# Kernel optimization log

Hardware: AMD Instinct MI355X
Metric: run time of the kernel (lower is better)

## Reference

```python
import jax, jax.numpy as jnp
import numpy as np

HIDDEN = 128
EDGE_DIM = 32
N_NODES = 50000
N_EDGES = 800000


def setup_inputs() -> dict:
    key = jax.random.key(0)
    ks = jax.random.split(key, 8)
    node_features = jax.random.normal(ks[0], (N_NODES, HIDDEN), dtype=jnp.float32)
    edge_index = jax.random.randint(ks[1], (2, N_EDGES), 0, N_NODES, dtype=jnp.int64)
    edge_attr = jax.random.normal(ks[2], (N_EDGES, EDGE_DIM), dtype=jnp.float32)
    # parameters (Linear stored as [in, out] for x @ W + b)
    s_et = 1.0 / np.sqrt(EDGE_DIM)
    W_edge = jax.random.uniform(ks[3], (EDGE_DIM, HIDDEN), jnp.float32, -s_et, s_et)
    b_edge = jnp.zeros((HIDDEN,), jnp.float32)
    s1 = 1.0 / np.sqrt(3 * HIDDEN)
    W1 = jax.random.uniform(ks[4], (3 * HIDDEN, HIDDEN), jnp.float32, -s1, s1)
    b1 = jnp.zeros((HIDDEN,), jnp.float32)
    s2 = 1.0 / np.sqrt(HIDDEN)
    W2 = jax.random.uniform(ks[5], (HIDDEN, 1), jnp.float32, -s2, s2)
    b2 = jnp.zeros((1,), jnp.float32)
    return {
        "node_features": node_features,
        "edge_attr": edge_attr,
        "W_edge": W_edge, "b_edge": b_edge,
        "W1": W1, "b1": b1, "W2": W2, "b2": b2,
        "edge_index": edge_index,
    }


def reference(node_features, edge_attr, W_edge, b_edge, W1, b1, W2, b2, edge_index):
    row, col = edge_index[0], edge_index[1]
    src = node_features[row]                 # [E, H] gather
    dst = node_features[col]                 # [E, H] gather
    edge_feat = edge_attr @ W_edge + b_edge  # [E, H]
    combined = jnp.concatenate([src, edge_feat, dst], axis=-1)  # [E, 3H]
    h = jax.nn.relu(combined @ W1 + b1)      # [E, H]
    attn = jax.nn.sigmoid(h @ W2 + b2)       # [E, 1]
    return attn
```

## Files before the change

### kernel.cpp

```cpp
#include <hip/hip_runtime.h>
#include <hip/hip_bf16.h>

#define HIDDEN   128
#define EDGE_DIM 32
#define NNODE    50000
#define NEDGE    800000
#define KSTEPS   9
#define NFRAG    8
#define LDS_KS   8

typedef __attribute__((ext_vector_type(4))) float        f32x4;
typedef __attribute__((ext_vector_type(8))) short        bf16x8;
typedef __attribute__((ext_vector_type(4))) unsigned int u32x4;

#define BPACK_USHORTS  (KSTEPS * NFRAG * 64 * 8)
#define BIAS_OFF_BYTES (BPACK_USHORTS * 2)
#define FLAG_OFF_BYTES (BIAS_OFF_BYTES + 128 * 4)
#define NODE_OFF_BYTES 74752
#define IDX_OFF_BYTES  (NODE_OFF_BYTES + NNODE * HIDDEN * 2)
#define WS_NEEDED      (IDX_OFF_BYTES + 2 * NEDGE * 4)

__device__ __forceinline__ unsigned short f2bf(float f) {
  unsigned u = __builtin_bit_cast(unsigned, f);
  u += 0x7FFFu + ((u >> 16) & 1u);
  return (unsigned short)(u >> 16);
}

__device__ __forceinline__ unsigned cvt_pk_bf16(float a, float b) {
  union { __hip_bfloat162 h; unsigned u; } cv;
  cv.h = __float22bfloat162_rn(make_float2(a, b));
  return cv.u;
}

__device__ __forceinline__ bf16x8 pack8(f32x4 lo, f32x4 hi) {
  u32x4 u;
  u[0] = cvt_pk_bf16(lo[0], lo[1]);
  u[1] = cvt_pk_bf16(lo[2], lo[3]);
  u[2] = cvt_pk_bf16(hi[0], hi[1]);
  u[3] = cvt_pk_bf16(hi[2], hi[3]);
  return __builtin_bit_cast(bf16x8, u);
}

__device__ __forceinline__ void gload_lds16(const void* g, void* l) {
  __builtin_amdgcn_global_load_lds(
      (const __attribute__((address_space(1))) unsigned int*)g,
      (__attribute__((address_space(3))) unsigned int*)l, 16, 0, 0);
}

#define MFMA(a, b, c) __builtin_amdgcn_mfma_f32_16x16x32_bf16((a), (b), (c), 0, 0, 0)

__global__ void setup_kernel(const float* __restrict__ W_edge,
                             const float* __restrict__ b_edge,
                             const float* __restrict__ W1,
                             const float* __restrict__ b1,
                             const void*  __restrict__ eidx,
                             unsigned short* __restrict__ Bpack,
                             float* __restrict__ bias_eff,
                             int*   __restrict__ flag64) {
  const int bid = blockIdx.x, tid = threadIdx.x;
  if (bid < 36) {
    const int pair  = bid * 2 + (tid >> 6);
    const int lane  = tid & 63;
    const int kstep = pair >> 3;
    const int f     = pair & 7;
    const int col   = f * 16 + (lane & 15);
    const int kbase = kstep * 32 + (lane >> 4) * 8;
    float vals[8];
#pragma unroll
    for (int j = 0; j < 8; ++j) {
      const int k = kbase + j;
      float val;
      if (k < 128) {
        val = W1[k * 128 + col];
      } else if (k < 256) {
        val = W1[(k + 128) * 128 + col];
      } else {
        const int kk = k - 256;
        float s = 0.f;
        for (int t = 0; t < 128; ++t)
          s = fmaf(W_edge[kk * 128 + t], W1[(128 + t) * 128 + col], s);
        val = s;
      }
      vals[j] = val;
    }
    u32x4 sv;
#pragma unroll
    for (int j = 0; j < 4; ++j)
      sv[j] = (unsigned)f2bf(vals[2 * j]) | ((unsigned)f2bf(vals[2 * j + 1]) << 16);
    *(u32x4*)(Bpack + ((kstep * NFRAG + f) * 64 + lane) * 8) = sv;
  } else {
    if (tid < 128) {
      float s = b1[tid];
      for (int t = 0; t < 128; ++t)
        s = fmaf(b_edge[t], W1[(128 + t) * 128 + tid], s);
      bias_eff[tid] = s;
    }
    if (tid == 0) {
      const unsigned* w = (const unsigned*)eidx;
      int all0 = 1;
      for (int i = 0; i < 64; ++i) all0 &= (w[2 * i + 1] == 0u) ? 1 : 0;
      *flag64 = all0;
    }
  }
}

__global__ __launch_bounds__(256) void cvt_nodes_kernel(const float* __restrict__ nodef,
                                                        unsigned short* __restrict__ nbf) {
  const int i = blockIdx.x * 256 + threadIdx.x;
  if (i >= NNODE * HIDDEN / 8) return;
  f32x4 lo = *(const f32x4*)(nodef + i * 8);
  f32x4 hi = *(const f32x4*)(nodef + i * 8 + 4);
  *(bf16x8*)(nbf + i * 8) = pack8(lo, hi);
}

__global__ __launch_bounds__(256) void cvt_idx_kernel(const void* __restrict__ eidx,
                                                      const int* __restrict__ flag64,
                                                      int* __restrict__ idx32) {
  const int i = blockIdx.x * 256 + threadIdx.x;
  if (i >= 2 * NEDGE) return;
  if (*flag64) idx32[i] = (int)((const long long*)eidx)[i];
  else         idx32[i] = ((const int*)eidx)[i];
}

__global__ __launch_bounds__(256, 2) void edge_attn_kernel(
    const unsigned short* __restrict__ nbf,
    const float* __restrict__ eattr,
    const int*   __restrict__ idx32,
    const unsigned short* __restrict__ Bpack,
    const float* __restrict__ bias_eff,
    const float* __restrict__ W2,
    const float* __restrict__ b2,
    float* __restrict__ out) {
  __shared__ unsigned short lds_b[LDS_KS * NFRAG * 64 * 8];

  const int tid   = threadIdx.x;
  const int lane  = tid & 63;
  const int wid   = tid >> 6;
  const int l15   = lane & 15;
  const int kg    = lane >> 4;
  const int ebase = blockIdx.x * 256 + wid * 64;

#pragma unroll
  for (int i = 0; i < 16; ++i) {
    const char* g = (const char*)Bpack + (size_t)(i * 256 + tid) * 16;
    char*       l = (char*)lds_b + (size_t)(i * 256 + wid * 64) * 16;
    gload_lds16(g, l);
  }

  int r[4], c[4];
#pragma unroll
  for (int mf = 0; mf < 4; ++mf) {
    r[mf] = idx32[ebase + mf * 16 + l15];
    c[mf] = idx32[NEDGE + ebase + mf * 16 + l15];
  }

  bf16x8 a[4][4];
#pragma unroll
  for (int mf = 0; mf < 4; ++mf)
#pragma unroll
    for (int ks = 0; ks < 4; ++ks)
      a[mf][ks] = *(const bf16x8*)(nbf + (size_t)r[mf] * HIDDEN + kg * 8 + ks * 32);

  __syncthreads();

  f32x4 acc[4][NFRAG];
#pragma unroll
  for (int mf = 0; mf < 4; ++mf)
#pragma unroll
    for (int f = 0; f < NFRAG; ++f)
      acc[mf][f] = (f32x4){0.f, 0.f, 0.f, 0.f};

#pragma unroll
  for (int ks = 0; ks < 4; ++ks)
#pragma unroll
    for (int f = 0; f < NFRAG; ++f) {
      bf16x8 bfr = *(const bf16x8*)(lds_b + ((ks * NFRAG + f) * 64 + lane) * 8);
#pragma unroll
      for (int mf = 0; mf < 4; ++mf)
        acc[mf][f] = MFMA(a[mf][ks], bfr, acc[mf][f]);
    }

  __builtin_amdgcn_sched_barrier(0);

#pragma unroll
  for (int mf = 0; mf < 4; ++mf)
#pragma unroll
    for (int ks = 0; ks < 4; ++ks)
      a[mf][ks] = *(const bf16x8*)(nbf + (size_t)c[mf] * HIDDEN + kg * 8 + ks * 32);

#pragma unroll
  for (int ks = 0; ks < 4; ++ks)
#pragma unroll
    for (int f = 0; f < NFRAG; ++f) {
      bf16x8 bfr = *(const bf16x8*)(lds_b + (((ks + 4) * NFRAG + f) * 64 + lane) * 8);
#pragma unroll
      for (int mf = 0; mf < 4; ++mf)
        acc[mf][f] = MFMA(a[mf][ks], bfr, acc[mf][f]);
    }

  __builtin_amdgcn_sched_barrier(0);

  bf16x8 ae[4];
#pragma unroll
  for (int mf = 0; mf < 4; ++mf) {
    const float* pe = eattr + (size_t)(ebase + mf * 16 + l15) * EDGE_DIM + kg * 8;
    f32x4 lo = *(const f32x4*)(pe);
    f32x4 hi = *(const f32x4*)(pe + 4);
    ae[mf] = pack8(lo, hi);
  }
#pragma unroll
  for (int f = 0; f < NFRAG; ++f) {
    bf16x8 bfr = *(const bf16x8*)(Bpack + ((8 * NFRAG + f) * 64 + lane) * 8);
#pragma unroll
    for (int mf = 0; mf < 4; ++mf)
      acc[mf][f] = MFMA(ae[mf], bfr, acc[mf][f]);
  }

  float w2v[NFRAG], bv[NFRAG];
#pragma unroll
  for (int f = 0; f < NFRAG; ++f) {
    w2v[f] = W2[f * 16 + l15];
    bv[f]  = bias_eff[f * 16 + l15];
  }
  const float bias2 = b2[0];

  float part[4][4];
#pragma unroll
  for (int mf = 0; mf < 4; ++mf)
#pragma unroll
    for (int rr = 0; rr < 4; ++rr) {
      float s = 0.f;
#pragma unroll
      for (int f = 0; f < NFRAG; ++f) {
        float h = fmaxf(acc[mf][f][rr] + bv[f], 0.f);
        s = fmaf(h, w2v[f], s);
      }
      part[mf][rr] = s;
    }

#pragma unroll
  for (int mask = 1; mask < 16; mask <<= 1)
#pragma unroll
    for (int mf = 0; mf < 4; ++mf)
#pragma unroll
      for (int rr = 0; rr < 4; ++rr)
        part[mf][rr] += __shfl_xor(part[mf][rr], mask, 64);

  if (l15 == 0) {
#pragma unroll
    for (int mf = 0; mf < 4; ++mf)
#pragma unroll
      for (int rr = 0; rr < 4; ++rr) {
        float x = part[mf][rr] + bias2;
        out[ebase + mf * 16 + kg * 4 + rr] = 1.f / (1.f + __expf(-x));
      }
  }
}

__global__ __launch_bounds__(256) void edge_attn_kernel_fp32(
    const float* __restrict__ nodef,
    const float* __restrict__ eattr,
    const void*  __restrict__ eidx,
    const unsigned short* __restrict__ Bpack,
    const float* __restrict__ bias_eff,
    const float* __restrict__ W2,
    const float* __restrict__ b2,
    const int*   __restrict__ flag64,
    float* __restrict__ out) {
  const int lane  = threadIdx.x & 63;
  const int wid   = threadIdx.x >> 6;
  const int ebase = blockIdx.x * 128 + wid * 32;
  const int l15   = lane & 15;
  const int kg    = lane >> 4;
  const int koff  = kg * 8;
  const int e0 = ebase + l15;
  const int e1 = e0 + 16;

  long r0, c0, r1, c1;
  if (*flag64) {
    const long long* p = (const long long*)eidx;
    r0 = (long)p[e0];          r1 = (long)p[e1];
    c0 = (long)p[NEDGE + e0];  c1 = (long)p[NEDGE + e1];
  } else {
    const int* p = (const int*)eidx;
    r0 = p[e0];          r1 = p[e1];
    c0 = p[NEDGE + e0];  c1 = p[NEDGE + e1];
  }

  f32x4 acc[2][NFRAG];
#pragma unroll
  for (int m = 0; m < 2; ++m)
#pragma unroll
    for (int f = 0; f < NFRAG; ++f)
      acc[m][f] = (f32x4){0.f, 0.f, 0.f, 0.f};

#pragma unroll 1
  for (int ks = 0; ks < KSTEPS; ++ks) {
    const float *p0, *p1;
    if (ks < 4)      { p0 = nodef + r0 * HIDDEN + ks * 32;       p1 = nodef + r1 * HIDDEN + ks * 32; }
    else if (ks < 8) { p0 = nodef + c0 * HIDDEN + (ks - 4) * 32; p1 = nodef + c1 * HIDDEN + (ks - 4) * 32; }
    else             { p0 = eattr + (long)e0 * EDGE_DIM;         p1 = eattr + (long)e1 * EDGE_DIM; }

    f32x4 lo0 = *(const f32x4*)(p0 + koff);
    f32x4 hi0 = *(const f32x4*)(p0 + koff + 4);
    f32x4 lo1 = *(const f32x4*)(p1 + koff);
    f32x4 hi1 = *(const f32x4*)(p1 + koff + 4);
    bf16x8 a0 = pack8(lo0, hi0);
    bf16x8 a1 = pack8(lo1, hi1);

#pragma unroll
    for (int f = 0; f < NFRAG; ++f) {
      bf16x8 bfr = *(const bf16x8*)(Bpack + ((ks * NFRAG + f) * 64 + lane) * 8);
      acc[0][f] = MFMA(a0, bfr, acc[0][f]);
      acc[1][f] = MFMA(a1, bfr, acc[1][f]);
    }
  }

  float w2v[NFRAG], bv[NFRAG];
#pragma unroll
  for (int f = 0; f < NFRAG; ++f) {
    w2v[f] = W2[f * 16 + l15];
    bv[f]  = bias_eff[f * 16 + l15];
  }
  const float bias2 = b2[0];

  float part[2][4];
#pragma unroll
  for (int m = 0; m < 2; ++m)
#pragma unroll
    for (int r = 0; r < 4; ++r) {
      float s = 0.f;
#pragma unroll
      for (int f = 0; f < NFRAG; ++f) {
        float h = acc[m][f][r] + bv[f];
        h = fmaxf(h, 0.f);
        s = fmaf(h, w2v[f], s);
      }
      part[m][r] = s;
    }

#pragma unroll
  for (int mask = 1; mask < 16; mask <<= 1)
#pragma unroll
    for (int m = 0; m < 2; ++m)
#pragma unroll
      for (int r = 0; r < 4; ++r)
        part[m][r] += __shfl_xor(part[m][r], mask, 64);

  if (l15 == 0) {
#pragma unroll
    for (int m = 0; m < 2; ++m)
#pragma unroll
      for (int r = 0; r < 4; ++r) {
        float x = part[m][r] + bias2;
        out[ebase + m * 16 + kg * 4 + r] = 1.f / (1.f + __expf(-x));
      }
  }
}

extern "C" void kernel_launch(void* const* d_in, const int* in_sizes, int n_in,
                              void* d_out, int out_size, void* d_ws, size_t ws_size,
                              hipStream_t stream) {
  const float* nodef  = (const float*)d_in[0];
  const float* eattr  = (const float*)d_in[1];
  const float* W_edge = (const float*)d_in[2];
  const float* b_edge = (const float*)d_in[3];
  const float* W1     = (const float*)d_in[4];
  const float* b1     = (const float*)d_in[5];
  const float* W2     = (const float*)d_in[6];
  const float* b2     = (const float*)d_in[7];
  const void*  eidx   = d_in[8];

  unsigned short* Bpack    = (unsigned short*)d_ws;
  float*          bias_eff = (float*)((char*)d_ws + BIAS_OFF_BYTES);
  int*            flag64   = (int*)((char*)d_ws + FLAG_OFF_BYTES);
  unsigned short* nbf      = (unsigned short*)((char*)d_ws + NODE_OFF_BYTES);
  int*            idx32    = (int*)((char*)d_ws + IDX_OFF_BYTES);

  setup_kernel<<<dim3(37), dim3(128), 0, stream>>>(W_edge, b_edge, W1, b1, eidx,
                                                   Bpack, bias_eff, flag64);

  if (ws_size >= (size_t)WS_NEEDED) {
    cvt_idx_kernel<<<dim3((2 * NEDGE + 255) / 256), dim3(256), 0, stream>>>(eidx, flag64, idx32);
    cvt_nodes_kernel<<<dim3((NNODE * HIDDEN / 8 + 255) / 256), dim3(256), 0, stream>>>(nodef, nbf);
    edge_attn_kernel<<<dim3(NEDGE / 256), dim3(256), 0, stream>>>(
        nbf, eattr, idx32, Bpack, bias_eff, W2, b2, (float*)d_out);
  } else {
    edge_attn_kernel_fp32<<<dim3(NEDGE / 128), dim3(256), 0, stream>>>(
        nodef, eattr, eidx, Bpack, bias_eff, W2, b2, flag64, (float*)d_out);
  }
}
```

Before: 132.4 us.

## Use 512-thread blocks with 32 edges per wave to raise occupancy

The main edge kernel now launches 512 threads per block, with each wave handling 32 edges (two M fragments) instead of 64. This halves the accumulator and A-fragment registers per thread, so launch bounds can target four blocks per CU and more waves can hide the latency of the gathers. The LDS copy of B is now spread across twice as many threads. In exchange, each B fragment read from LDS is reused by fewer MFMAs, so LDS traffic per edge doubles.

```diff
diff --git a/kernel.cpp b/kernel.cpp
--- a/kernel.cpp
+++ b/kernel.cpp
@@ -122,7 +122,7 @@
   else         idx32[i] = ((const int*)eidx)[i];
 }
 
-__global__ __launch_bounds__(256, 2) void edge_attn_kernel(
+__global__ __launch_bounds__(512, 4) void edge_attn_kernel(
     const unsigned short* __restrict__ nbf,
     const float* __restrict__ eattr,
     const int*   __restrict__ idx32,
@@ -138,82 +138,82 @@
   const int wid   = tid >> 6;
   const int l15   = lane & 15;
   const int kg    = lane >> 4;
-  const int ebase = blockIdx.x * 256 + wid * 64;
-
-#pragma unroll
-  for (int i = 0; i < 16; ++i) {
-    const char* g = (const char*)Bpack + (size_t)(i * 256 + tid) * 16;
-    char*       l = (char*)lds_b + (size_t)(i * 256 + wid * 64) * 16;
+  const int ebase = blockIdx.x * 256 + wid * 32;
+
+#pragma unroll
+  for (int i = 0; i < 8; ++i) {
+    const char* g = (const char*)Bpack + (size_t)(i * 512 + tid) * 16;
+    char*       l = (char*)lds_b + (size_t)(i * 512 + wid * 64) * 16;
     gload_lds16(g, l);
   }
 
-  int r[4], c[4];
-#pragma unroll
-  for (int mf = 0; mf < 4; ++mf) {
-    r[mf] = idx32[ebase + mf * 16 + l15];
-    c[mf] = idx32[NEDGE + ebase + mf * 16 + l15];
-  }
-
-  bf16x8 a[4][4];
-#pragma unroll
-  for (int mf = 0; mf < 4; ++mf)
-#pragma unroll
-    for (int ks = 0; ks < 4; ++ks)
-      a[mf][ks] = *(const bf16x8*)(nbf + (size_t)r[mf] * HIDDEN + kg * 8 + ks * 32);
+  const int r0 = idx32[ebase + l15];
+  const int r1 = idx32[ebase + 16 + l15];
+  const int c0 = idx32[NEDGE + ebase + l15];
+  const int c1 = idx32[NEDGE + ebase + 16 + l15];
+
+  bf16x8 a0[4], a1[4];
+#pragma unroll
+  for (int ks = 0; ks < 4; ++ks) {
+    a0[ks] = *(const bf16x8*)(nbf + (size_t)r0 * HIDDEN + kg * 8 + ks * 32);
+    a1[ks] = *(const bf16x8*)(nbf + (size_t)r1 * HIDDEN + kg * 8 + ks * 32);
+  }
 
   __syncthreads();
 
-  f32x4 acc[4][NFRAG];
-#pragma unroll
-  for (int mf = 0; mf < 4; ++mf)
+  f32x4 acc[2][NFRAG];
+#pragma unroll
+  for (int m = 0; m < 2; ++m)
 #pragma unroll
     for (int f = 0; f < NFRAG; ++f)
-      acc[mf][f] = (f32x4){0.f, 0.f, 0.f, 0.f};
+      acc[m][f] = (f32x4){0.f, 0.f, 0.f, 0.f};
 
 #pragma unroll
   for (int ks = 0; ks < 4; ++ks)
 #pragma unroll
     for (int f = 0; f < NFRAG; ++f) {
       bf16x8 bfr = *(const bf16x8*)(lds_b + ((ks * NFRAG + f) * 64 + lane) * 8);
-#pragma unroll
-      for (int mf = 0; mf < 4; ++mf)
-        acc[mf][f] = MFMA(a[mf][ks], bfr, acc[mf][f]);
+      acc[0][f] = MFMA(a0[ks], bfr, acc[0][f]);
+      acc[1][f] = MFMA(a1[ks], bfr, acc[1][f]);
     }
 
   __builtin_amdgcn_sched_barrier(0);
 
 #pragma unroll
-  for (int mf = 0; mf < 4; ++mf)
-#pragma unroll
-    for (int ks = 0; ks < 4; ++ks)
-      a[mf][ks] = *(const bf16x8*)(nbf + (size_t)c[mf] * HIDDEN + kg * 8 + ks * 32);
+  for (int ks = 0; ks < 4; ++ks) {
+    a0[ks] = *(const bf16x8*)(nbf + (size_t)c0 * HIDDEN + kg * 8 + ks * 32);
+    a1[ks] = *(const bf16x8*)(nbf + (size_t)c1 * HIDDEN + kg * 8 + ks * 32);
+  }
 
 #pragma unroll
   for (int ks = 0; ks < 4; ++ks)
 #pragma unroll
     for (int f = 0; f < NFRAG; ++f) {
       bf16x8 bfr = *(const bf16x8*)(lds_b + (((ks + 4) * NFRAG + f) * 64 + lane) * 8);
-#pragma unroll
-      for (int mf = 0; mf < 4; ++mf)
-        acc[mf][f] = MFMA(a[mf][ks], bfr, acc[mf][f]);
+      acc[0][f] = MFMA(a0[ks], bfr, acc[0][f]);
+      acc[1][f] = MFMA(a1[ks], bfr, acc[1][f]);
     }
 
   __builtin_amdgcn_sched_barrier(0);
 
-  bf16x8 ae[4];
-#pragma unroll
-  for (int mf = 0; mf < 4; ++mf) {
-    const float* pe = eattr + (size_t)(ebase + mf * 16 + l15) * EDGE_DIM + kg * 8;
+  bf16x8 ae0, ae1;
+  {
+    const float* pe = eattr + (size_t)(ebase + l15) * EDGE_DIM + kg * 8;
     f32x4 lo = *(const f32x4*)(pe);
     f32x4 hi = *(const f32x4*)(pe + 4);
-    ae[mf] = pack8(lo, hi);
+    ae0 = pack8(lo, hi);
+  }
+  {
+    const float* pe = eattr + (size_t)(ebase + 16 + l15) * EDGE_DIM + kg * 8;
+    f32x4 lo = *(const f32x4*)(pe);
+    f32x4 hi = *(const f32x4*)(pe + 4);
+    ae1 = pack8(lo, hi);
   }
 #pragma unroll
   for (int f = 0; f < NFRAG; ++f) {
     bf16x8 bfr = *(const bf16x8*)(Bpack + ((8 * NFRAG + f) * 64 + lane) * 8);
-#pragma unroll
-    for (int mf = 0; mf < 4; ++mf)
-      acc[mf][f] = MFMA(ae[mf], bfr, acc[mf][f]);
+    acc[0][f] = MFMA(ae0, bfr, acc[0][f]);
+    acc[1][f] = MFMA(ae1, bfr, acc[1][f]);
   }
 
   float w2v[NFRAG], bv[NFRAG];
@@ -224,35 +224,35 @@
   }
   const float bias2 = b2[0];
 
-  float part[4][4];
-#pragma unroll
-  for (int mf = 0; mf < 4; ++mf)
+  float part[2][4];
+#pragma unroll
+  for (int m = 0; m < 2; ++m)
 #pragma unroll
     for (int rr = 0; rr < 4; ++rr) {
       float s = 0.f;
 #pragma unroll
       for (int f = 0; f < NFRAG; ++f) {
-        float h = fmaxf(acc[mf][f][rr] + bv[f], 0.f);
+        float h = fmaxf(acc[m][f][rr] + bv[f], 0.f);
         s = fmaf(h, w2v[f], s);
       }
-      part[mf][rr] = s;
+      part[m][rr] = s;
     }
 
 #pragma unroll
   for (int mask = 1; mask < 16; mask <<= 1)
 #pragma unroll
-    for (int mf = 0; mf < 4; ++mf)
+    for (int m = 0; m < 2; ++m)
 #pragma unroll
       for (int rr = 0; rr < 4; ++rr)
-        part[mf][rr] += __shfl_xor(part[mf][rr], mask, 64);
+        part[m][rr] += __shfl_xor(part[m][rr], mask, 64);
 
   if (l15 == 0) {
 #pragma unroll
-    for (int mf = 0; mf < 4; ++mf)
+    for (int m = 0; m < 2; ++m)
 #pragma unroll
       for (int rr = 0; rr < 4; ++rr) {
-        float x = part[mf][rr] + bias2;
-        out[ebase + mf * 16 + kg * 4 + rr] = 1.f / (1.f + __expf(-x));
+        float x = part[m][rr] + bias2;
+        out[ebase + m * 16 + kg * 4 + rr] = 1.f / (1.f + __expf(-x));
       }
   }
 }
@@ -383,7 +383,7 @@
   if (ws_size >= (size_t)WS_NEEDED) {
     cvt_idx_kernel<<<dim3((2 * NEDGE + 255) / 256), dim3(256), 0, stream>>>(eidx, flag64, idx32);
     cvt_nodes_kernel<<<dim3((NNODE * HIDDEN / 8 + 255) / 256), dim3(256), 0, stream>>>(nodef, nbf);
-    edge_attn_kernel<<<dim3(NEDGE / 256), dim3(256), 0, stream>>>(
+    edge_attn_kernel<<<dim3(NEDGE / 256), dim3(512), 0, stream>>>(
         nbf, eattr, idx32, Bpack, bias_eff, W2, b2, (float*)d_out);
   } else {
     edge_attn_kernel_fp32<<<dim3(NEDGE / 128), dim3(256), 0, stream>>>(
```

After: 128.8 us. 2.7% less time.
